# Kernel tuning notes

Measured on AMD Instinct MI355X. Metric: run time of the kernel, lower is better.

The kernel has to match this reference:

```python
import jax, jax.numpy as jnp
import numpy as np

S, B, H = 4096, 1, 2048       # [seq, batch, hidden] layout (NeoX convention)
NP, HN = 16, H // 16          # heads, head dim
ROT = int(HN * 0.25)          # rotary_ndims = 32 (rotary_pct=0.25)
ROPE_BASE = 10000.0


def setup_inputs() -> dict:
    key = jax.random.key(0)
    k0, k1, k2 = jax.random.split(key, 3)
    hidden_states = jax.random.normal(k0, (S, B, H), jnp.float32) * 0.02
    # causal left-to-right mask: True = masked out (filled with -10000)
    attention_mask = jnp.triu(jnp.ones((1, 1, S, S), bool), k=1)
    w_qkv = jax.random.normal(k1, (3 * H, H), jnp.float32) * (1.0 / np.sqrt(H))
    w_dense = jax.random.normal(k2, (H, H), jnp.float32) * (1.0 / np.sqrt(H))
    b_dense = jnp.zeros((H,), jnp.float32)
    return {"hidden_states": hidden_states, "attention_mask": attention_mask,
            "w_qkv": w_qkv, "w_dense": w_dense, "b_dense": b_dense}


def _apply_rope(x, pos):
    # x: [s, b, np, ROT]; NeoX rotate_half convention
    inv_freq = 1.0 / (ROPE_BASE ** (jnp.arange(0, ROT, 2, dtype=jnp.float32) / ROT))
    freqs = pos[:, None] * inv_freq[None, :]              # [s, ROT/2]
    emb = jnp.concatenate([freqs, freqs], axis=-1)        # [s, ROT]
    cos = jnp.cos(emb)[:, None, None, :]
    sin = jnp.sin(emb)[:, None, None, :]
    x1, x2 = jnp.split(x, 2, axis=-1)
    rot = jnp.concatenate([-x2, x1], axis=-1)
    return x * cos + rot * sin


def reference(hidden_states, attention_mask, w_qkv, w_dense, b_dense):
    s, b, h = hidden_states.shape
    # fused QKV projection (no bias), reshape to [s, b, np, 3*hn], split
    qkv = (hidden_states @ w_qkv.T).reshape(s, b, NP, 3 * HN)
    q, k, v = jnp.split(qkv, 3, axis=-1)                  # each [s, b, np, hn]
    # partial rotary embedding on first ROT dims
    pos = jnp.arange(s, dtype=jnp.float32)
    q = jnp.concatenate([_apply_rope(q[..., :ROT], pos), q[..., ROT:]], axis=-1)
    k = jnp.concatenate([_apply_rope(k[..., :ROT], pos), k[..., ROT:]], axis=-1)
    # raw attention scores [b, np, s_q, s_k], scale 1/sqrt(hn)
    scores = jnp.einsum('sbhd,tbhd->bhst', q, k) / np.float32(np.sqrt(HN))
    # ltor mask: fill masked positions with -10000, softmax in fp32
    scores = jnp.where(attention_mask, jnp.float32(-10000.0), scores)
    probs = jax.nn.softmax(scores.astype(jnp.float32), axis=-1).astype(hidden_states.dtype)
    # context [s, b, np, hn] -> [s, b, h]
    ctx = jnp.einsum('bhst,tbhd->sbhd', probs, v).reshape(s, b, h)
    return ctx @ w_dense.T + b_dense
```

## Files before the change

### kernel.cpp

```cpp
#include <hip/hip_runtime.h>

#define S_LEN 4096
#define HID   2048
#define NHEAD 16
#define HDIM  128
#define QSCALE_L2E 0.12751664352f

typedef float  f32x4  __attribute__((ext_vector_type(4)));
typedef float  f32x16 __attribute__((ext_vector_type(16)));
typedef __bf16 bf16x8 __attribute__((ext_vector_type(8)));
typedef unsigned u32x4 __attribute__((ext_vector_type(4)));
typedef unsigned u32x2 __attribute__((ext_vector_type(2)));

#define MFMA16(a, b, c) __builtin_amdgcn_mfma_f32_16x16x32_bf16((a), (b), (c), 0, 0, 0)
#define MFMA32(a, b, c) __builtin_amdgcn_mfma_f32_32x32x16_bf16((a), (b), (c), 0, 0, 0)

__device__ __forceinline__ void gld16(const void* g, void* l) {
  __builtin_amdgcn_global_load_lds(
      (const __attribute__((address_space(1))) void*)(unsigned long long)(g),
      (__attribute__((address_space(3))) void*)(unsigned long long)(l),
      16, 0, 0);
}

__device__ __forceinline__ unsigned short f2bf(float f) {
  union { float f; unsigned u; } v; v.f = f;
  unsigned r = v.u + 0x7FFFu + ((v.u >> 16) & 1u);
  return (unsigned short)(r >> 16);
}
__device__ __forceinline__ float bf2f(unsigned short h) {
  union { unsigned u; float f; } v; v.u = ((unsigned)h) << 16;
  return v.f;
}
__device__ __forceinline__ unsigned cvtpk_bf16(float a, float b) {
  unsigned r;
  asm("v_cvt_pk_bf16_f32 %0, %1, %2" : "=v"(r) : "v"(a), "v"(b));
  return r;
}
__device__ __forceinline__ u32x2 pls(unsigned a, unsigned b) {
  return __builtin_amdgcn_permlane32_swap(a, b, false, false);
}
__device__ __forceinline__ float asf(unsigned u) { return __builtin_bit_cast(float, u); }
__device__ __forceinline__ unsigned asu(float f) { return __builtin_bit_cast(unsigned, f); }

__global__ __launch_bounds__(256) void cvt_kernel(const float* __restrict__ src,
                                                  unsigned short* __restrict__ dst, int n) {
  int i = (blockIdx.x * 256 + threadIdx.x) * 4;
  if (i >= n) return;
  const float4 v = *(const float4*)(src + i);
  ushort4 o;
  o.x = f2bf(v.x); o.y = f2bf(v.y); o.z = f2bf(v.z); o.w = f2bf(v.w);
  *(ushort4*)(dst + i) = o;
}

template <int EPI>
__global__ __launch_bounds__(512, 2) void gemm256_kernel(
    const unsigned short* __restrict__ A, const unsigned short* __restrict__ B,
    unsigned short* __restrict__ Qb, unsigned short* __restrict__ Kb,
    unsigned short* __restrict__ Vt,
    const float* __restrict__ bias, float* __restrict__ out) {
  __shared__ __align__(16) unsigned char sm[98304];
  constexpr int K = HID;
  constexpr int NT = K / 64;
  constexpr int NB = (EPI == 0) ? 768 : 256;
  const int b = (int)blockIdx.x;
  const int swz = (b & 7) * (NB >> 3) + (b >> 3);
  const int bm = swz & 15, bn = swz >> 4;
  const int row0 = bm * 256, col0 = bn * 128;
  const int tid = threadIdx.x;
  const int wid = tid >> 6, lane = tid & 63;
  const int g = lane >> 4, r16 = lane & 15;
  const int wm = wid >> 1, wn = wid & 1;

  auto stageA = [&](int t) {
    const int bufo = (t & 1) * 49152;
    const int k0 = t * 64;
#pragma unroll
    for (int h = 0; h < 2; ++h)
#pragma unroll
      for (int cc = 0; cc < 2; ++cc) {
        const int chunk = cc * 512 + tid;
        const int r = chunk >> 3, c7 = chunk & 7;
        gld16(A + (row0 + h * 128 + r) * K + k0 + ((c7 ^ (r & 7)) << 3),
              sm + bufo + h * 16384 + chunk * 16);
      }
  };
  auto stageB = [&](int t) {
    const int bufo = (t & 1) * 49152;
    const int k0 = t * 64;
#pragma unroll
    for (int cc = 0; cc < 2; ++cc) {
      const int chunk = cc * 512 + tid;
      const int r = chunk >> 3, c7 = chunk & 7;
      gld16(B + (col0 + r) * K + k0 + ((c7 ^ (r & 7)) << 3),
            sm + bufo + 32768 + chunk * 16);
    }
  };

  f32x4 acc[4][4] = {};

  int aoff[4], boff[4];
#pragma unroll
  for (int m = 0; m < 4; ++m) {
    const int r = (wm & 1) * 64 + m * 16 + r16;
    aoff[m] = (wm >> 1) * 16384 + r * 128 + ((g * 16) ^ ((r & 7) << 4));
  }
#pragma unroll
  for (int n = 0; n < 4; ++n) {
    const int r = wn * 64 + n * 16 + r16;
    boff[n] = 32768 + r * 128 + ((g * 16) ^ ((r & 7) << 4));
  }

  stageA(0); stageB(0);
  asm volatile("s_waitcnt vmcnt(0)" ::: "memory");
  __builtin_amdgcn_s_barrier();

  for (int t = 0; t < NT; ++t) {
    const int bufo = (t & 1) * 49152;
    const bool st = (t + 1 < NT);
    bf16x8 af[4], bfv[4];
#pragma unroll
    for (int m = 0; m < 4; ++m) af[m] = *(const bf16x8*)(sm + bufo + aoff[m]);
#pragma unroll
    for (int n = 0; n < 4; ++n) bfv[n] = *(const bf16x8*)(sm + bufo + boff[n]);
    if (st) stageA(t + 1);
    __builtin_amdgcn_s_barrier();
    asm volatile("s_waitcnt lgkmcnt(0)" ::: "memory");
    __builtin_amdgcn_s_setprio(1);
#pragma unroll
    for (int m = 0; m < 4; ++m)
#pragma unroll
      for (int n = 0; n < 4; ++n) acc[m][n] = MFMA16(af[m], bfv[n], acc[m][n]);
    __builtin_amdgcn_s_setprio(0);
    __builtin_amdgcn_s_barrier();
#pragma unroll
    for (int m = 0; m < 4; ++m) af[m] = *(const bf16x8*)(sm + bufo + (aoff[m] ^ 64));
#pragma unroll
    for (int n = 0; n < 4; ++n) bfv[n] = *(const bf16x8*)(sm + bufo + (boff[n] ^ 64));
    if (st) stageB(t + 1);
    __builtin_amdgcn_s_barrier();
    asm volatile("s_waitcnt lgkmcnt(0)" ::: "memory");
    __builtin_amdgcn_s_setprio(1);
#pragma unroll
    for (int m = 0; m < 4; ++m)
#pragma unroll
      for (int n = 0; n < 4; ++n) acc[m][n] = MFMA16(af[m], bfv[n], acc[m][n]);
    __builtin_amdgcn_s_setprio(0);
    if (st) asm volatile("s_waitcnt vmcnt(0)" ::: "memory");
    __builtin_amdgcn_s_barrier();
  }

  if constexpr (EPI == 0) {
    const int type = bn % 3, p = bn / 3;
#pragma unroll
    for (int m = 0; m < 4; ++m) {
      const int s0 = row0 + wm * 64 + m * 16 + g * 4;
#pragma unroll
      for (int n = 0; n < 4; ++n) {
        const int d = wn * 64 + n * 16 + r16;
        if (type == 0) {
#pragma unroll
          for (int r = 0; r < 4; ++r)
            Qb[(p * S_LEN + s0 + r) * HDIM + d] = f2bf(acc[m][n][r] * QSCALE_L2E);
        } else if (type == 1) {
#pragma unroll
          for (int r = 0; r < 4; ++r)
            Kb[(p * S_LEN + s0 + r) * HDIM + d] = f2bf(acc[m][n][r]);
        } else {
          ushort4 o;
          o.x = f2bf(acc[m][n][0]); o.y = f2bf(acc[m][n][1]);
          o.z = f2bf(acc[m][n][2]); o.w = f2bf(acc[m][n][3]);
          *(ushort4*)(Vt + (p * HDIM + d) * S_LEN + s0) = o;
        }
      }
    }
  } else {
#pragma unroll
    for (int m = 0; m < 4; ++m) {
      const int s0 = row0 + wm * 64 + m * 16 + g * 4;
#pragma unroll
      for (int n = 0; n < 4; ++n) {
        const int col = col0 + wn * 64 + n * 16 + r16;
        const float bv = bias[col];
#pragma unroll
        for (int r = 0; r < 4; ++r)
          out[(s0 + r) * HID + col] = acc[m][n][r] + bv;
      }
    }
  }
}

__global__ __launch_bounds__(256) void rope_kernel(unsigned short* __restrict__ Qb,
                                                   unsigned short* __restrict__ Kb) {
  const int idx = blockIdx.x * 256 + threadIdx.x;
  const int p = idx >> 16, rem = idx & 65535, s = rem >> 4, d = rem & 15;
  const float invf = exp2f(-(float)d * (13.287712379549449f / 16.0f));
  const float ang = (float)s * invf;
  const float c = cosf(ang), sn = sinf(ang);
  const int base = (p * S_LEN + s) * HDIM;
  {
    float x = bf2f(Qb[base + d]), y = bf2f(Qb[base + d + 16]);
    Qb[base + d]      = f2bf(x * c - y * sn);
    Qb[base + d + 16] = f2bf(y * c + x * sn);
  }
  {
    float x = bf2f(Kb[base + d]), y = bf2f(Kb[base + d + 16]);
    Kb[base + d]      = f2bf(x * c - y * sn);
    Kb[base + d + 16] = f2bf(y * c + x * sn);
  }
}

__global__ __launch_bounds__(256, 2) void attn_kernel(
    const unsigned short* __restrict__ Qb, const unsigned short* __restrict__ Kb,
    const unsigned short* __restrict__ Vt, unsigned short* __restrict__ Ctx) {
  __shared__ __align__(16) unsigned char sm[81920];
  const int b = (int)blockIdx.x;
  const int p = b & 15;
  const int qt = (b < 256) ? (b >> 4) : 47 - (b >> 4);
  const int tid = threadIdx.x, wid = tid >> 6, lane = tid & 63;
  const int l31 = lane & 31, hi = lane >> 5;
  const int xr = (l31 & 7) << 4;

  const int q0w = qt * 128 + wid * 32;
  const int qg = q0w + l31;
  const int nt = 2 * (qt + 1);
  const int np = nt >> 1;

  auto stage = [&](int t, int ko, int vo) {
    const unsigned short* kb = Kb + (p * S_LEN + t * 64) * HDIM;
    const unsigned short* vb = Vt + p * HDIM * S_LEN + t * 64;
#pragma unroll
    for (int c = 0; c < 4; ++c) {
      const int chunk = c * 256 + tid;
      const int byteoff = chunk * 16;
      const int j = byteoff >> 8, cbK = (byteoff >> 4) & 15;
      gld16(kb + j * HDIM + (cbK ^ (j & 7)) * 8, sm + ko + chunk * 16);
      const int dd = byteoff >> 7, cbV = (byteoff >> 4) & 7;
      gld16(vb + dd * S_LEN + (cbV ^ (dd & 7)) * 8, sm + vo + chunk * 16);
    }
  };

  bf16x8 qf[8];
  f32x16 acc[4] = {};
  float m_s = -1e30f, l_s = 0.f;

  auto qk = [&](f32x16& s0, f32x16& s1, const unsigned char* kl) {
    __builtin_amdgcn_s_setprio(1);
#pragma unroll
    for (int dd = 0; dd < 8; ++dd) {
      bf16x8 k0 = *(const bf16x8*)(kl + l31 * 256 + (((dd * 2 + hi) << 4) ^ xr));
      bf16x8 k1 = *(const bf16x8*)(kl + (32 + l31) * 256 + (((dd * 2 + hi) << 4) ^ xr));
      s0 = MFMA32(k0, qf[dd], s0);
      s1 = MFMA32(k1, qf[dd], s1);
    }
    __builtin_amdgcn_s_setprio(0);
  };

  auto smpv = [&](f32x16& s0, f32x16& s1, int t, int vo) {
    const unsigned char* vl = sm + vo;
    if (t * 64 + 63 > q0w) {
#pragma unroll
      for (int r = 0; r < 16; ++r) {
        const int kv0 = t * 64 + ((r & 3) + 8 * (r >> 2)) + 4 * hi;
        if (kv0 > qg) s0[r] = -1e30f;
        if (kv0 + 32 > qg) s1[r] = -1e30f;
      }
    }
    float mx[16];
#pragma unroll
    for (int r = 0; r < 16; ++r) mx[r] = fmaxf(s0[r], s1[r]);
#pragma unroll
    for (int r = 0; r < 8; ++r) mx[r] = fmaxf(mx[r], mx[r + 8]);
#pragma unroll
    for (int r = 0; r < 4; ++r) mx[r] = fmaxf(mx[r], mx[r + 4]);
    mx[0] = fmaxf(fmaxf(mx[0], mx[2]), fmaxf(mx[1], mx[3]));
    float pm;
    {
      u32x2 e = pls(asu(mx[0]), asu(mx[0]));
      pm = fmaxf(asf(e.x), asf(e.y));
    }
    if (__any(pm > m_s + 11.5f)) {
      const float mn = fmaxf(m_s, pm);
      const float scl = exp2f(m_s - mn);
#pragma unroll
      for (int d32 = 0; d32 < 4; ++d32)
#pragma unroll
        for (int r = 0; r < 16; ++r) acc[d32][r] *= scl;
      l_s *= scl;
      m_s = mn;
    }
#pragma unroll
    for (int r = 0; r < 16; ++r) {
      s0[r] = exp2f(s0[r] - m_s);
      s1[r] = exp2f(s1[r] - m_s);
    }
    bf16x8 pf[4];
#define PACKB(B, SV, base)                                                        \
    {                                                                             \
      unsigned X0 = cvtpk_bf16(SV[base + 0], SV[base + 1]);                       \
      unsigned X1 = cvtpk_bf16(SV[base + 2], SV[base + 3]);                       \
      unsigned Y0 = cvtpk_bf16(SV[base + 4], SV[base + 5]);                       \
      unsigned Y1 = cvtpk_bf16(SV[base + 6], SV[base + 7]);                       \
      u32x2 e0 = pls(X0, Y0);                                                     \
      u32x2 e1 = pls(X1, Y1);                                                     \
      u32x4 pw;                                                                   \
      pw.x = e0.x; pw.y = e1.x; pw.z = e0.y; pw.w = e1.y;                         \
      pf[B] = __builtin_bit_cast(bf16x8, pw);                                     \
    }
    PACKB(0, s0, 0)
    PACKB(1, s0, 8)
    PACKB(2, s1, 0)
    PACKB(3, s1, 8)
#undef PACKB
    __builtin_amdgcn_s_setprio(1);
#pragma unroll
    for (int d32 = 0; d32 < 4; ++d32) {
#pragma unroll
      for (int bb = 0; bb < 4; ++bb) {
        bf16x8 vf = *(const bf16x8*)(vl + (d32 * 32 + l31) * 128 + (((bb * 2 + hi) << 4) ^ xr));
        acc[d32] = MFMA32(vf, pf[bb], acc[d32]);
      }
    }
    __builtin_amdgcn_s_setprio(0);
    float s_[8];
#pragma unroll
    for (int r = 0; r < 8; ++r) s_[r] = (s0[r] + s0[r + 8]) + (s1[r] + s1[r + 8]);
#pragma unroll
    for (int r = 0; r < 4; ++r) s_[r] += s_[r + 4];
    const float rs = (s_[0] + s_[1]) + (s_[2] + s_[3]);
    u32x2 e = pls(asu(rs), asu(rs));
    l_s += asf(e.x) + asf(e.y);
  };

  stage(0, 0, 32768);
  stage(1, 16384, 49152);
  {
    const unsigned short* qp_ = Qb + (p * S_LEN + qg) * HDIM + hi * 8;
#pragma unroll
    for (int dd = 0; dd < 8; ++dd) qf[dd] = *(const bf16x8*)(qp_ + dd * 16);
  }
  int vcur = 32768, vnext = 49152, vstage = 65536;
  __syncthreads();
  f32x16 sA0 = {}, sA1 = {};
  qk(sA0, sA1, sm);
  __syncthreads();

  for (int tt = 0; tt < np; ++tt) {
    const bool more = (tt + 1 < np);
    const int t = 2 * tt;
    f32x16 sB0 = {}, sB1 = {};
    qk(sB0, sB1, sm + 16384);
    if (more) stage(t + 2, 0, vstage);
    smpv(sA0, sA1, t, vcur);
    { int tmp = vcur; vcur = vnext; vnext = vstage; vstage = tmp; }
    __syncthreads();
    if (more) {
      sA0 = {}; sA1 = {};
      qk(sA0, sA1, sm);
      stage(t + 3, 16384, vstage);
    }
    smpv(sB0, sB1, t + 1, vcur);
    { int tmp = vcur; vcur = vnext; vnext = vstage; vstage = tmp; }
    __syncthreads();
  }

  const float inv = 1.0f / l_s;
  unsigned short* cbase = Ctx + qg * HID + p * HDIM;
#pragma unroll
  for (int d32 = 0; d32 < 4; ++d32)
#pragma unroll
    for (int r = 0; r < 16; ++r) {
      const int d = d32 * 32 + ((r & 3) + 8 * (r >> 2)) + 4 * hi;
      cbase[d] = f2bf(acc[d32][r] * inv);
    }
}

extern "C" void kernel_launch(void* const* d_in, const int* in_sizes, int n_in,
                              void* d_out, int out_size, void* d_ws, size_t ws_size,
                              hipStream_t stream) {
  (void)in_sizes; (void)n_in; (void)out_size; (void)ws_size;
  const float* hidden = (const float*)d_in[0];
  const float* wqkv   = (const float*)d_in[2];
  const float* wdense = (const float*)d_in[3];
  const float* bdense = (const float*)d_in[4];
  float* out = (float*)d_out;

  char* ws = (char*)d_ws;
  unsigned short* hiddenB = (unsigned short*)(ws);
  unsigned short* wqkvB   = (unsigned short*)(ws + 16777216);
  unsigned short* wdenseB = (unsigned short*)(ws + 41943040);
  unsigned short* Qb      = (unsigned short*)(ws + 50331648);
  unsigned short* Kb      = (unsigned short*)(ws + 67108864);
  unsigned short* Vt      = (unsigned short*)(ws + 83886080);
  unsigned short* ctxB    = (unsigned short*)(ws + 100663296);

  cvt_kernel<<<8192, 256, 0, stream>>>(hidden, hiddenB, 8388608);
  cvt_kernel<<<12288, 256, 0, stream>>>(wqkv, wqkvB, 12582912);
  cvt_kernel<<<4096, 256, 0, stream>>>(wdense, wdenseB, 4194304);
  gemm256_kernel<0><<<768, 512, 0, stream>>>(hiddenB, wqkvB, Qb, Kb, Vt, nullptr, nullptr);
  rope_kernel<<<4096, 256, 0, stream>>>(Qb, Kb);
  attn_kernel<<<512, 256, 0, stream>>>(Qb, Kb, Vt, ctxB);
  gemm256_kernel<1><<<256, 512, 0, stream>>>(ctxB, wdenseB, nullptr, nullptr, nullptr, bdense, out);
}
```

Before: 316.2 us.

## Triple-buffer GEMM, fuse RoPE into QKV epilogue, retune attention staging and waits

The GEMM moves from double to triple buffering with a prefetch distance of two and partial vmcnt waits, which removes the mid-iteration barriers. Shared memory grows to 144KB, which likely limits the kernel to one block per CU. The separate rope kernel is deleted and rotary is applied in the QKV GEMM epilogue, saving a launch and a read-modify-write pass over Q and K. The attention kernel gets a new 16-way swizzled K/V LDS layout and explicit partial vmcnt waits instead of __syncthreads. The Q fragment loads are also hoisted ahead of the K/V staging.

```diff
diff --git a/kernel.cpp b/kernel.cpp
--- a/kernel.cpp
+++ b/kernel.cpp
@@ -58,7 +58,7 @@
     unsigned short* __restrict__ Qb, unsigned short* __restrict__ Kb,
     unsigned short* __restrict__ Vt,
     const float* __restrict__ bias, float* __restrict__ out) {
-  __shared__ __align__(16) unsigned char sm[98304];
+  __shared__ __align__(16) unsigned char sm[147456];
   constexpr int K = HID;
   constexpr int NT = K / 64;
   constexpr int NB = (EPI == 0) ? 768 : 256;
@@ -71,8 +71,7 @@
   const int g = lane >> 4, r16 = lane & 15;
   const int wm = wid >> 1, wn = wid & 1;
 
-  auto stageA = [&](int t) {
-    const int bufo = (t & 1) * 49152;
+  auto stageA = [&](int t, int bufo) {
     const int k0 = t * 64;
 #pragma unroll
     for (int h = 0; h < 2; ++h)
@@ -84,8 +83,7 @@
               sm + bufo + h * 16384 + chunk * 16);
       }
   };
-  auto stageB = [&](int t) {
-    const int bufo = (t & 1) * 49152;
+  auto stageB = [&](int t, int bufo) {
     const int k0 = t * 64;
 #pragma unroll
     for (int cc = 0; cc < 2; ++cc) {
@@ -110,62 +108,85 @@
     boff[n] = 32768 + r * 128 + ((g * 16) ^ ((r & 7) << 4));
   }
 
-  stageA(0); stageB(0);
-  asm volatile("s_waitcnt vmcnt(0)" ::: "memory");
+  stageA(0, 0); stageB(0, 0);
+  stageA(1, 49152); stageB(1, 49152);
+  asm volatile("s_waitcnt vmcnt(6)" ::: "memory");
   __builtin_amdgcn_s_barrier();
-
+  __builtin_amdgcn_sched_barrier(0);
+
+  int curo = 0, stgo = 98304;
   for (int t = 0; t < NT; ++t) {
-    const int bufo = (t & 1) * 49152;
-    const bool st = (t + 1 < NT);
+    const bool st = (t + 2 < NT);
     bf16x8 af[4], bfv[4];
 #pragma unroll
-    for (int m = 0; m < 4; ++m) af[m] = *(const bf16x8*)(sm + bufo + aoff[m]);
-#pragma unroll
-    for (int n = 0; n < 4; ++n) bfv[n] = *(const bf16x8*)(sm + bufo + boff[n]);
-    if (st) stageA(t + 1);
-    __builtin_amdgcn_s_barrier();
-    asm volatile("s_waitcnt lgkmcnt(0)" ::: "memory");
+    for (int m = 0; m < 4; ++m) af[m] = *(const bf16x8*)(sm + curo + aoff[m]);
+#pragma unroll
+    for (int n = 0; n < 4; ++n) bfv[n] = *(const bf16x8*)(sm + curo + boff[n]);
+    if (st) stageA(t + 2, stgo);
     __builtin_amdgcn_s_setprio(1);
 #pragma unroll
     for (int m = 0; m < 4; ++m)
 #pragma unroll
       for (int n = 0; n < 4; ++n) acc[m][n] = MFMA16(af[m], bfv[n], acc[m][n]);
     __builtin_amdgcn_s_setprio(0);
-    __builtin_amdgcn_s_barrier();
-#pragma unroll
-    for (int m = 0; m < 4; ++m) af[m] = *(const bf16x8*)(sm + bufo + (aoff[m] ^ 64));
-#pragma unroll
-    for (int n = 0; n < 4; ++n) bfv[n] = *(const bf16x8*)(sm + bufo + (boff[n] ^ 64));
-    if (st) stageB(t + 1);
-    __builtin_amdgcn_s_barrier();
-    asm volatile("s_waitcnt lgkmcnt(0)" ::: "memory");
+#pragma unroll
+    for (int m = 0; m < 4; ++m) af[m] = *(const bf16x8*)(sm + curo + (aoff[m] ^ 64));
+#pragma unroll
+    for (int n = 0; n < 4; ++n) bfv[n] = *(const bf16x8*)(sm + curo + (boff[n] ^ 64));
+    if (st) stageB(t + 2, stgo);
     __builtin_amdgcn_s_setprio(1);
 #pragma unroll
     for (int m = 0; m < 4; ++m)
 #pragma unroll
       for (int n = 0; n < 4; ++n) acc[m][n] = MFMA16(af[m], bfv[n], acc[m][n]);
     __builtin_amdgcn_s_setprio(0);
-    if (st) asm volatile("s_waitcnt vmcnt(0)" ::: "memory");
+    if (st) asm volatile("s_waitcnt vmcnt(6)" ::: "memory");
+    else    asm volatile("s_waitcnt vmcnt(0)" ::: "memory");
     __builtin_amdgcn_s_barrier();
+    __builtin_amdgcn_sched_barrier(0);
+    curo = (curo == 98304) ? 0 : curo + 49152;
+    stgo = (stgo == 98304) ? 0 : stgo + 49152;
   }
 
   if constexpr (EPI == 0) {
     const int type = bn % 3, p = bn / 3;
-#pragma unroll
-    for (int m = 0; m < 4; ++m) {
-      const int s0 = row0 + wm * 64 + m * 16 + g * 4;
-#pragma unroll
-      for (int n = 0; n < 4; ++n) {
-        const int d = wn * 64 + n * 16 + r16;
-        if (type == 0) {
-#pragma unroll
-          for (int r = 0; r < 4; ++r)
-            Qb[(p * S_LEN + s0 + r) * HDIM + d] = f2bf(acc[m][n][r] * QSCALE_L2E);
-        } else if (type == 1) {
-#pragma unroll
-          for (int r = 0; r < 4; ++r)
-            Kb[(p * S_LEN + s0 + r) * HDIM + d] = f2bf(acc[m][n][r]);
+    if (type <= 1) {
+      unsigned short* Ob = (type == 0) ? Qb : Kb;
+      const float qs = (type == 0) ? QSCALE_L2E : 1.0f;
+      const float invf = exp2f(-(float)r16 * 0.8304820237218406f);
+#pragma unroll
+      for (int m = 0; m < 4; ++m) {
+        const int s0 = row0 + wm * 64 + m * 16 + g * 4;
+        if (wn == 0) {
+#pragma unroll
+          for (int r = 0; r < 4; ++r) {
+            const float ang = (float)(s0 + r) * invf;
+            const float c = cosf(ang), sn = sinf(ang);
+            const float x = acc[m][0][r] * qs, y = acc[m][1][r] * qs;
+            unsigned short* dst = Ob + (p * S_LEN + s0 + r) * HDIM;
+            dst[r16]      = f2bf(x * c - y * sn);
+            dst[16 + r16] = f2bf(y * c + x * sn);
+          }
+#pragma unroll
+          for (int n = 2; n < 4; ++n)
+#pragma unroll
+            for (int r = 0; r < 4; ++r)
+              Ob[(p * S_LEN + s0 + r) * HDIM + n * 16 + r16] = f2bf(acc[m][n][r] * qs);
         } else {
+#pragma unroll
+          for (int n = 0; n < 4; ++n)
+#pragma unroll
+            for (int r = 0; r < 4; ++r)
+              Ob[(p * S_LEN + s0 + r) * HDIM + 64 + n * 16 + r16] = f2bf(acc[m][n][r] * qs);
+        }
+      }
+    } else {
+#pragma unroll
+      for (int m = 0; m < 4; ++m) {
+        const int s0 = row0 + wm * 64 + m * 16 + g * 4;
+#pragma unroll
+        for (int n = 0; n < 4; ++n) {
+          const int d = wn * 64 + n * 16 + r16;
           ushort4 o;
           o.x = f2bf(acc[m][n][0]); o.y = f2bf(acc[m][n][1]);
           o.z = f2bf(acc[m][n][2]); o.w = f2bf(acc[m][n][3]);
@@ -186,26 +207,6 @@
           out[(s0 + r) * HID + col] = acc[m][n][r] + bv;
       }
     }
-  }
-}
-
-__global__ __launch_bounds__(256) void rope_kernel(unsigned short* __restrict__ Qb,
-                                                   unsigned short* __restrict__ Kb) {
-  const int idx = blockIdx.x * 256 + threadIdx.x;
-  const int p = idx >> 16, rem = idx & 65535, s = rem >> 4, d = rem & 15;
-  const float invf = exp2f(-(float)d * (13.287712379549449f / 16.0f));
-  const float ang = (float)s * invf;
-  const float c = cosf(ang), sn = sinf(ang);
-  const int base = (p * S_LEN + s) * HDIM;
-  {
-    float x = bf2f(Qb[base + d]), y = bf2f(Qb[base + d + 16]);
-    Qb[base + d]      = f2bf(x * c - y * sn);
-    Qb[base + d + 16] = f2bf(y * c + x * sn);
-  }
-  {
-    float x = bf2f(Kb[base + d]), y = bf2f(Kb[base + d + 16]);
-    Kb[base + d]      = f2bf(x * c - y * sn);
-    Kb[base + d + 16] = f2bf(y * c + x * sn);
   }
 }
 
@@ -218,7 +219,7 @@
   const int qt = (b < 256) ? (b >> 4) : 47 - (b >> 4);
   const int tid = threadIdx.x, wid = tid >> 6, lane = tid & 63;
   const int l31 = lane & 31, hi = lane >> 5;
-  const int xr = (l31 & 7) << 4;
+  const int xr = (l31 & 15) << 4;
 
   const int q0w = qt * 128 + wid * 32;
   const int qg = q0w + l31;
@@ -230,12 +231,16 @@
     const unsigned short* vb = Vt + p * HDIM * S_LEN + t * 64;
 #pragma unroll
     for (int c = 0; c < 4; ++c) {
-      const int chunk = c * 256 + tid;
-      const int byteoff = chunk * 16;
-      const int j = byteoff >> 8, cbK = (byteoff >> 4) & 15;
-      gld16(kb + j * HDIM + (cbK ^ (j & 7)) * 8, sm + ko + chunk * 16);
-      const int dd = byteoff >> 7, cbV = (byteoff >> 4) & 7;
-      gld16(vb + dd * S_LEN + (cbV ^ (dd & 7)) * 8, sm + vo + chunk * 16);
+      const int ch = c * 256 + tid;
+      const int j = ch >> 4, cb = ch & 15;
+      gld16(kb + j * HDIM + ((cb ^ (j & 15)) << 3), sm + ko + ch * 16);
+    }
+#pragma unroll
+    for (int c = 0; c < 4; ++c) {
+      const int ch = c * 256 + tid;
+      const int r = ch >> 4, cb = ch & 15;
+      const int lc = cb ^ (r & 15);
+      gld16(vb + (r + ((lc >> 3) << 6)) * S_LEN + ((lc & 7) << 3), sm + vo + ch * 16);
     }
   };
 
@@ -314,9 +319,11 @@
     __builtin_amdgcn_s_setprio(1);
 #pragma unroll
     for (int d32 = 0; d32 < 4; ++d32) {
+      const int row = (d32 & 1) * 32 + l31;
+      const int ho = (d32 >> 1) * 128;
 #pragma unroll
       for (int bb = 0; bb < 4; ++bb) {
-        bf16x8 vf = *(const bf16x8*)(vl + (d32 * 32 + l31) * 128 + (((bb * 2 + hi) << 4) ^ xr));
+        bf16x8 vf = *(const bf16x8*)(vl + row * 256 + ((ho + ((bb * 2 + hi) << 4)) ^ xr));
         acc[d32] = MFMA32(vf, pf[bb], acc[d32]);
       }
     }
@@ -331,18 +338,21 @@
     l_s += asf(e.x) + asf(e.y);
   };
 
+  {
+    const unsigned short* qp_ = Qb + (p * S_LEN + qg) * HDIM + hi * 8;
+#pragma unroll
+    for (int dd = 0; dd < 8; ++dd) qf[dd] = *(const bf16x8*)(qp_ + dd * 16);
+  }
   stage(0, 0, 32768);
   stage(1, 16384, 49152);
-  {
-    const unsigned short* qp_ = Qb + (p * S_LEN + qg) * HDIM + hi * 8;
-#pragma unroll
-    for (int dd = 0; dd < 8; ++dd) qf[dd] = *(const bf16x8*)(qp_ + dd * 16);
-  }
   int vcur = 32768, vnext = 49152, vstage = 65536;
-  __syncthreads();
+  asm volatile("s_waitcnt vmcnt(0)" ::: "memory");
+  __builtin_amdgcn_s_barrier();
+  __builtin_amdgcn_sched_barrier(0);
   f32x16 sA0 = {}, sA1 = {};
   qk(sA0, sA1, sm);
-  __syncthreads();
+  __builtin_amdgcn_s_barrier();
+  __builtin_amdgcn_sched_barrier(0);
 
   for (int tt = 0; tt < np; ++tt) {
     const bool more = (tt + 1 < np);
@@ -352,7 +362,10 @@
     if (more) stage(t + 2, 0, vstage);
     smpv(sA0, sA1, t, vcur);
     { int tmp = vcur; vcur = vnext; vnext = vstage; vstage = tmp; }
-    __syncthreads();
+    if (more) asm volatile("s_waitcnt vmcnt(4)" ::: "memory");
+    else      asm volatile("s_waitcnt vmcnt(0)" ::: "memory");
+    __builtin_amdgcn_s_barrier();
+    __builtin_amdgcn_sched_barrier(0);
     if (more) {
       sA0 = {}; sA1 = {};
       qk(sA0, sA1, sm);
@@ -360,7 +373,10 @@
     }
     smpv(sB0, sB1, t + 1, vcur);
     { int tmp = vcur; vcur = vnext; vnext = vstage; vstage = tmp; }
-    __syncthreads();
+    if (more) asm volatile("s_waitcnt vmcnt(4)" ::: "memory");
+    else      asm volatile("s_waitcnt vmcnt(0)" ::: "memory");
+    __builtin_amdgcn_s_barrier();
+    __builtin_amdgcn_sched_barrier(0);
   }
 
   const float inv = 1.0f / l_s;
@@ -397,7 +413,6 @@
   cvt_kernel<<<12288, 256, 0, stream>>>(wqkv, wqkvB, 12582912);
   cvt_kernel<<<4096, 256, 0, stream>>>(wdense, wdenseB, 4194304);
   gemm256_kernel<0><<<768, 512, 0, stream>>>(hiddenB, wqkvB, Qb, Kb, Vt, nullptr, nullptr);
-  rope_kernel<<<4096, 256, 0, stream>>>(Qb, Kb);
   attn_kernel<<<512, 256, 0, stream>>>(Qb, Kb, Vt, ctxB);
   gemm256_kernel<1><<<256, 512, 0, stream>>>(ctxB, wdenseB, nullptr, nullptr, nullptr, bdense, out);
 }
```

Measured after the change: 319.5 us. No clear change (+1.0%).
